# Performance work log

Hardware: AMD Instinct MI355X
Metric: run time of the kernel (lower is better)

Reference implementation:

```python
import jax, jax.numpy as jnp
import numpy as np

D_MODEL = 1024
NUM_HEADS = 16
DEPTH = D_MODEL // NUM_HEADS  # 64
BATCH, SEQ = 4, 2048


def setup_inputs() -> dict:
    key = jax.random.key(0)
    ks = jax.random.split(key, 9)
    s = 1.0 / np.sqrt(D_MODEL)
    x = jax.random.normal(ks[0], (BATCH, SEQ, D_MODEL), dtype=jnp.float32)
    # Per-head Dense weights stacked on a leading head axis [H, d_model, depth]
    Wq = jax.random.normal(ks[1], (NUM_HEADS, D_MODEL, DEPTH), dtype=jnp.float32) * s
    Wk = jax.random.normal(ks[2], (NUM_HEADS, D_MODEL, DEPTH), dtype=jnp.float32) * s
    Wv = jax.random.normal(ks[3], (NUM_HEADS, D_MODEL, DEPTH), dtype=jnp.float32) * s
    bq = jnp.zeros((NUM_HEADS, DEPTH), dtype=jnp.float32)
    bk = jnp.zeros((NUM_HEADS, DEPTH), dtype=jnp.float32)
    bv = jnp.zeros((NUM_HEADS, DEPTH), dtype=jnp.float32)
    Wo = jax.random.normal(ks[4], (D_MODEL, D_MODEL), dtype=jnp.float32) * s
    bo = jnp.zeros((D_MODEL,), dtype=jnp.float32)
    return {"x": x, "Wq": Wq, "bq": bq, "Wk": Wk, "bk": bk,
            "Wv": Wv, "bv": bv, "Wo": Wo, "bo": bo}


def reference(x, Wq, bq, Wk, bk, Wv, bv, Wo, bo):
    # Batched equivalent of the per-head loop: project, attend, concat heads.
    q = jnp.einsum('bsd,hde->bhse', x, Wq) + bq[:, None, :]  # [B,H,S,depth]
    k = jnp.einsum('bsd,hde->bhse', x, Wk) + bk[:, None, :]
    v = jnp.einsum('bsd,hde->bhse', x, Wv) + bv[:, None, :]
    scale = 1.0 / jnp.sqrt(jnp.asarray(DEPTH, dtype=x.dtype))
    scores = jnp.einsum('bhse,bhte->bhst', q, k) * scale      # [B,H,S,S]
    weights = jax.nn.softmax(scores, axis=-1)
    heads = jnp.einsum('bhst,bhte->bhse', weights, v)         # [B,H,S,depth]
    # concat head outputs along last axis in head order (tf.concat axis=-1)
    multi = jnp.transpose(heads, (0, 2, 1, 3)).reshape(x.shape[0], x.shape[1], D_MODEL)
    return multi @ Wo + bo
```

## Files before the change

kernel.cpp:

```cpp
#include <hip/hip_runtime.h>
#include <hip/hip_bf16.h>

#define BATCH 4
#define SEQ   2048
#define DM    1024
#define NH    16
#define DEPTH 64
#define ROWS  (BATCH*SEQ)
#define NQKV  (3*DM)
#define BH    (BATCH*NH)

typedef __attribute__((ext_vector_type(8))) short bf16x8;
typedef __attribute__((ext_vector_type(4))) float f32x4;
typedef __attribute__((ext_vector_type(16))) float f32x16;
typedef unsigned short u16;
typedef unsigned int   u32;

__device__ __forceinline__ u16 f2bf(float f) {
    union { float f; unsigned u; } v; v.f = f;
    unsigned r = v.u + 0x7fff + ((v.u >> 16) & 1);
    return (u16)(r >> 16);
}

__device__ __forceinline__ u32 pk2bf(float a, float b) {
#if __has_builtin(__builtin_amdgcn_cvt_pk_bf16_f32)
    typedef __attribute__((ext_vector_type(2))) __bf16 v2bf;
    union { v2bf v; u32 u; } u_;
    u_.v = __builtin_amdgcn_cvt_pk_bf16_f32(a, b);
    return u_.u;
#else
    return (u32)f2bf(a) | ((u32)f2bf(b) << 16);
#endif
}

__device__ __forceinline__ void plswap(u32 a, u32 b, u32& x, u32& y) {
#if __has_builtin(__builtin_amdgcn_permlane32_swap)
    typedef __attribute__((ext_vector_type(2))) int i32x2;
    i32x2 r = __builtin_amdgcn_permlane32_swap((int)a, (int)b, false, false);
    x = (u32)r.x; y = (u32)r.y;
#else
    u32 as = (u32)__shfl_xor((int)a, 32);
    u32 bs = (u32)__shfl_xor((int)b, 32);
    int h = (threadIdx.x >> 5) & 1;
    x = h ? bs : a;
    y = h ? b : as;
#endif
}

__device__ __forceinline__ void g2l16(void* lds, const void* g) {
    __builtin_amdgcn_global_load_lds((const __attribute__((address_space(1))) void*)g,
                                     (__attribute__((address_space(3))) void*)lds, 16, 0, 0);
}

__device__ __forceinline__ bf16x8 frag8(const u16* tile, int row, int gl) {
    return *(const bf16x8*)(tile + row * 64 + ((gl ^ (row & 7)) * 8));
}

__device__ __forceinline__ f32x16 mfma32(bf16x8 a, bf16x8 b, f32x16 c) {
    return __builtin_amdgcn_mfma_f32_32x32x16_bf16(a, b, c, 0, 0, 0);
}

__global__ __launch_bounds__(256) void k_prep(const float* __restrict__ x,
                                              const float* __restrict__ Wq, const float* __restrict__ Wk,
                                              const float* __restrict__ Wv, const float* __restrict__ Wo,
                                              u16* __restrict__ xb, u16* __restrict__ BT, u16* __restrict__ WoT) {
    __shared__ u16 T[64][65];
    int tid = threadIdx.x;
    int bx = blockIdx.x;
    if (bx < 2048) {
        int i = bx * 4096 + tid * 4;
        for (int l = 0; l < 4; ++l) {
            float4 v = *(const float4*)(x + i + l * 1024);
            ushort4 o; o.x = f2bf(v.x); o.y = f2bf(v.y); o.z = f2bf(v.z); o.w = f2bf(v.w);
            *(ushort4*)(xb + i + l * 1024) = o;
        }
        return;
    }
    if (bx < 2816) {
        int q = bx - 2048;
        int kt = q & 15, mh = q >> 4, m = mh >> 4, h = mh & 15;
        const float* W = (m == 0) ? Wq : (m == 1) ? Wk : Wv;
        const float* src = W + ((size_t)h * 1024 + kt * 64) * 64;
        int e = tid & 63, r0 = tid >> 6;
        for (int i = 0; i < 16; ++i) { int r = i * 4 + r0; T[r][e] = f2bf(src[r * 64 + e]); }
        __syncthreads();
        int kk = tid & 63, e0 = tid >> 6;
        u16* dst = BT + ((size_t)m * 1024 + h * 64) * 1024 + kt * 64;
        for (int i = 0; i < 16; ++i) { int ee = i * 4 + e0; dst[ee * 1024 + kk] = T[kk][ee]; }
        return;
    }
    {
        int q = bx - 2816;
        int kt = q & 15, nt = q >> 4;
        const float* src = Wo + (size_t)kt * 64 * 1024 + nt * 64;
        int c = tid & 63, r0 = tid >> 6;
        for (int i = 0; i < 16; ++i) { int r = i * 4 + r0; T[r][c] = f2bf(src[r * 1024 + c]); }
        __syncthreads();
        int kk = tid & 63, e0 = tid >> 6;
        u16* dst = WoT + (size_t)nt * 64 * 1024 + kt * 64;
        for (int i = 0; i < 16; ++i) { int ee = i * 4 + e0; dst[ee * 1024 + kk] = T[kk][ee]; }
    }
}

__global__ __launch_bounds__(256, 2) void k_gemm_qkv(const u16* __restrict__ xb, const u16* __restrict__ Wt,
                                                     const float* __restrict__ bq, const float* __restrict__ bk,
                                                     const float* __restrict__ bv,
                                                     u16* __restrict__ Q, u16* __restrict__ K, u16* __restrict__ VT) {
    __shared__ u16 Al[2][128 * 64];
    __shared__ u16 Bl[2][128 * 64];
    int tid = threadIdx.x;
    int wave = tid >> 6, lane = tid & 63, l31 = lane & 31, h2 = lane >> 5;
    int wr = wave >> 1, wc = wave & 1;

    int b = blockIdx.x;
    int wg = (b & 7) * 192 + (b >> 3);

    bool isvt = (wg >= 1024);
    int row0, col0;
    const u16 *Am, *Bm;
    if (!isvt) {
        row0 = (wg >> 4) * 128; col0 = (wg & 15) * 128;
        Am = xb + (size_t)row0 * 1024;
        Bm = Wt + (size_t)col0 * 1024;
    } else {
        int b2 = wg - 1024;
        row0 = (b2 >> 6) * 128; col0 = (b2 & 63) * 128;
        Am = Wt + (size_t)(2048 + row0) * 1024;
        Bm = xb + (size_t)col0 * 1024;
    }

    f32x16 acc[2][2] = {};

    int sr[4], sgs[4], sdst[4];
#pragma unroll
    for (int l = 0; l < 4; ++l) {
        int idx = tid + l * 256;
        sr[l] = idx >> 3; sgs[l] = ((idx & 7) ^ (sr[l] & 7)) * 8; sdst[l] = idx * 8;
    }

#define QKV_STAGE(bufi, k0) \
    { _Pragma("unroll") for (int l = 0; l < 4; ++l) { \
        g2l16(&Al[bufi][sdst[l]], Am + sr[l] * 1024 + (k0) + sgs[l]); \
        g2l16(&Bl[bufi][sdst[l]], Bm + sr[l] * 1024 + (k0) + sgs[l]); } }

#define QKV_COMPUTE(bufi) \
    { _Pragma("unroll") for (int kk = 0; kk < 4; ++kk) { \
        bf16x8 a_[2], bb_[2]; \
        _Pragma("unroll") for (int mi = 0; mi < 2; ++mi) a_[mi] = frag8(Al[bufi], wr * 64 + mi * 32 + l31, 2 * kk + h2); \
        _Pragma("unroll") for (int ni = 0; ni < 2; ++ni) bb_[ni] = frag8(Bl[bufi], wc * 64 + ni * 32 + l31, 2 * kk + h2); \
        _Pragma("unroll") for (int mi = 0; mi < 2; ++mi) \
        _Pragma("unroll") for (int ni = 0; ni < 2; ++ni) \
            acc[mi][ni] = mfma32(a_[mi], bb_[ni], acc[mi][ni]); } }

    QKV_STAGE(0, 0)
    QKV_STAGE(1, 64)

    for (int t = 0; t < 15; ++t) {
        int cur = t & 1;
        asm volatile("s_waitcnt vmcnt(8)" ::: "memory");
        __builtin_amdgcn_s_barrier();
        asm volatile("" ::: "memory");
        __builtin_amdgcn_s_setprio(1);
        QKV_COMPUTE(cur)
        __builtin_amdgcn_s_setprio(0);
        asm volatile("" ::: "memory");
        __builtin_amdgcn_s_barrier();
        if (t < 14) QKV_STAGE(cur, (t + 2) * 64)
    }
    asm volatile("s_waitcnt vmcnt(0)" ::: "memory");
    __builtin_amdgcn_s_barrier();
    asm volatile("" ::: "memory");
    QKV_COMPUTE(1)
#undef QKV_STAGE
#undef QKV_COMPUTE

    if (!isvt) {
        const float QSCALE = 0.125f * 1.4426950408889634f;
        int m = (col0 >= 1024);
        const float* bias = m ? bk : bq;
        u16* dst0 = m ? K : Q;
#pragma unroll
        for (int ni = 0; ni < 2; ++ni) {
            int c = col0 + wc * 64 + ni * 32 + l31;
            int h = (c >> 6) & 15, e = c & 63;
            float bval = bias[h * 64 + e];
#pragma unroll
            for (int mi = 0; mi < 2; ++mi)
#pragma unroll
                for (int reg = 0; reg < 16; ++reg) {
                    int rowg = row0 + wr * 64 + mi * 32 + (reg & 3) + 8 * (reg >> 2) + 4 * h2;
                    int b_ = rowg >> 11, s = rowg & 2047;
                    int bh = b_ * 16 + h;
                    float v = acc[mi][ni][reg] + bval;
                    if (!m) v *= QSCALE;
                    dst0[((size_t)bh * 2048 + s) * 64 + e] = f2bf(v);
                }
        }
    } else {
#pragma unroll
        for (int ni = 0; ni < 2; ++ni) {
            int c = col0 + wc * 64 + ni * 32 + l31;
            int b_ = c >> 11, s = c & 2047;
#pragma unroll
            for (int mi = 0; mi < 2; ++mi)
#pragma unroll
                for (int reg = 0; reg < 16; ++reg) {
                    int ii = row0 + wr * 64 + mi * 32 + (reg & 3) + 8 * (reg >> 2) + 4 * h2;
                    float v = acc[mi][ni][reg] + bv[ii];
                    VT[((size_t)b_ * 1024 + ii) * 2048 + s] = f2bf(v);
                }
        }
    }
}

__global__ __launch_bounds__(256, 4) void k_attn(const u16* __restrict__ Q, const u16* __restrict__ K,
                                                 const u16* __restrict__ VT, u16* __restrict__ A2) {
    __shared__ u16 Kl[2][64 * 64];
    __shared__ u16 Vl[2][64 * 64];
    __shared__ float linv[128];
    int tid = threadIdx.x;
    int wave = tid >> 6, lane = tid & 63, l31 = lane & 31, h = lane >> 5;
    int bh = blockIdx.y;
    int m0 = blockIdx.x * 128;
    const u16* Qb = Q + (size_t)bh * 2048 * 64;
    const u16* Kb = K + (size_t)bh * 2048 * 64;
    const u16* Vb = VT + (size_t)bh * 64 * 2048;

    const u16* kp[2]; const u16* vp[2]; int dsti[2];
    for (int l = 0; l < 2; ++l) {
        int idx = tid + l * 256, r = idx >> 3, gs = ((idx & 7) ^ (r & 7)) * 8;
        dsti[l] = idx * 8;
        kp[l] = Kb + r * 64 + gs;
        vp[l] = Vb + r * 2048 + gs;
    }

    bf16x8 qb[4];
    {
        const u16* q0 = Qb + (size_t)(m0 + wave * 32 + l31) * 64 + h * 8;
#pragma unroll
        for (int s = 0; s < 4; ++s) qb[s] = *(const bf16x8*)(q0 + s * 16);
    }

    for (int l = 0; l < 2; ++l) { g2l16(&Kl[0][dsti[l]], kp[l]); g2l16(&Vl[0][dsti[l]], vp[l]); }
    asm volatile("s_waitcnt vmcnt(0)" ::: "memory");
    __builtin_amdgcn_s_barrier();
    asm volatile("" ::: "memory");

    f32x16 oacc[2] = {};
    float lsum = 0.f;
    bf16x8 pa[4] = {};

    for (int t = 0; t < 32; ++t) {
        int cur = t & 1, nxt = cur ^ 1;

        if (t < 31) {
            for (int l = 0; l < 2; ++l) g2l16(&Kl[nxt][dsti[l]], kp[l] + (t + 1) * 4096);
        }

        f32x16 sc[2] = {};
        __builtin_amdgcn_s_setprio(1);
#pragma unroll
        for (int s = 0; s < 4; ++s) {
            bf16x8 kf0 = frag8(Kl[cur], l31,      2 * s + h);
            bf16x8 kf1 = frag8(Kl[cur], 32 + l31, 2 * s + h);
            sc[0] = mfma32(kf0, qb[s], sc[0]);
            sc[1] = mfma32(kf1, qb[s], sc[1]);
        }
        if (t > 0) {
#pragma unroll
            for (int s = 0; s < 4; ++s) {
                bf16x8 bv0 = frag8(Vl[nxt], l31,      2 * s + h);
                bf16x8 bv1 = frag8(Vl[nxt], 32 + l31, 2 * s + h);
                oacc[0] = mfma32(pa[s], bv0, oacc[0]);
                oacc[1] = mfma32(pa[s], bv1, oacc[1]);
            }
        }
        __builtin_amdgcn_s_setprio(0);

        asm volatile("" ::: "memory");
        __builtin_amdgcn_s_barrier();
        asm volatile("" ::: "memory");

        if (t < 31) {
            for (int l = 0; l < 2; ++l) g2l16(&Vl[nxt][dsti[l]], vp[l] + (t + 1) * 64);
        }

        float sq = 0.f;
#pragma unroll
        for (int kt = 0; kt < 2; ++kt)
#pragma unroll
            for (int gp = 0; gp < 2; ++gp) {
                float e00 = __builtin_amdgcn_exp2f(sc[kt][(2 * gp) * 4 + 0]);
                float e01 = __builtin_amdgcn_exp2f(sc[kt][(2 * gp) * 4 + 1]);
                float e02 = __builtin_amdgcn_exp2f(sc[kt][(2 * gp) * 4 + 2]);
                float e03 = __builtin_amdgcn_exp2f(sc[kt][(2 * gp) * 4 + 3]);
                float e10 = __builtin_amdgcn_exp2f(sc[kt][(2 * gp + 1) * 4 + 0]);
                float e11 = __builtin_amdgcn_exp2f(sc[kt][(2 * gp + 1) * 4 + 1]);
                float e12 = __builtin_amdgcn_exp2f(sc[kt][(2 * gp + 1) * 4 + 2]);
                float e13 = __builtin_amdgcn_exp2f(sc[kt][(2 * gp + 1) * 4 + 3]);
                sq += ((e00 + e01) + (e02 + e03)) + ((e10 + e11) + (e12 + e13));
                u32 ue = pk2bf(e00, e01), ve = pk2bf(e02, e03);
                u32 uo = pk2bf(e10, e11), vo = pk2bf(e12, e13);
                u32 w0, w1, w2, w3;
                plswap(ue, uo, w0, w2);
                plswap(ve, vo, w1, w3);
                union { bf16x8 v; u32 w[4]; } pu;
                pu.w[0] = w0; pu.w[1] = w1; pu.w[2] = w2; pu.w[3] = w3;
                pa[2 * kt + gp] = pu.v;
            }
        lsum += sq;

        if (t < 31) {
            asm volatile("s_waitcnt vmcnt(0)" ::: "memory");
            __builtin_amdgcn_s_barrier();
            asm volatile("" ::: "memory");
        }
    }

#pragma unroll
    for (int s = 0; s < 4; ++s) {
        bf16x8 bv0 = frag8(Vl[1], l31,      2 * s + h);
        bf16x8 bv1 = frag8(Vl[1], 32 + l31, 2 * s + h);
        oacc[0] = mfma32(pa[s], bv0, oacc[0]);
        oacc[1] = mfma32(pa[s], bv1, oacc[1]);
    }

    {
        float l2 = lsum + __shfl_xor(lsum, 32);
        linv[wave * 32 + l31] = 1.0f / l2;
    }
    int b_ = bh >> 4, hh = bh & 15;
    for (int g = 0; g < 4; ++g) {
        f32x4 iv = *(f32x4*)&linv[wave * 32 + 8 * g + 4 * h];
        for (int dt = 0; dt < 2; ++dt)
            for (int r = 0; r < 4; ++r) {
                int row = b_ * 2048 + m0 + wave * 32 + 8 * g + 4 * h + r;
                A2[row * 1024 + hh * 64 + dt * 32 + l31] = f2bf(oacc[dt][g * 4 + r] * iv[r]);
            }
    }
}

__global__ __launch_bounds__(256, 2) void k_gemm_out(const u16* __restrict__ A, const u16* __restrict__ BT,
                                                     const float* __restrict__ bo, float* __restrict__ out) {
    __shared__ u16 Al[2][128 * 64];
    __shared__ u16 Bl[2][128 * 64];
    int tid = threadIdx.x;
    int wave = tid >> 6, lane = tid & 63, l31 = lane & 31, h2 = lane >> 5;
    int wr = wave >> 1, wc = wave & 1;

    int b = blockIdx.x;
    int wg = (b & 7) * 64 + (b >> 3);
    int row0 = (wg >> 3) * 128, col0 = (wg & 7) * 128;

    const u16* Am = A  + (size_t)row0 * 1024;
    const u16* Bm = BT + (size_t)col0 * 1024;

    f32x16 acc[2][2] = {};

    int sr[4], sgs[4], sdst[4];
#pragma unroll
    for (int l = 0; l < 4; ++l) {
        int idx = tid + l * 256;
        sr[l] = idx >> 3; sgs[l] = ((idx & 7) ^ (sr[l] & 7)) * 8; sdst[l] = idx * 8;
    }

#define OUT_STAGE(bufi, k0) \
    { _Pragma("unroll") for (int l = 0; l < 4; ++l) { \
        g2l16(&Al[bufi][sdst[l]], Am + sr[l] * 1024 + (k0) + sgs[l]); \
        g2l16(&Bl[bufi][sdst[l]], Bm + sr[l] * 1024 + (k0) + sgs[l]); } }

#define OUT_COMPUTE(bufi) \
    { _Pragma("unroll") for (int kk = 0; kk < 4; ++kk) { \
        bf16x8 a_[2], bb_[2]; \
        _Pragma("unroll") for (int mi = 0; mi < 2; ++mi) a_[mi] = frag8(Al[bufi], wr * 64 + mi * 32 + l31, 2 * kk + h2); \
        _Pragma("unroll") for (int ni = 0; ni < 2; ++ni) bb_[ni] = frag8(Bl[bufi], wc * 64 + ni * 32 + l31, 2 * kk + h2); \
        _Pragma("unroll") for (int mi = 0; mi < 2; ++mi) \
        _Pragma("unroll") for (int ni = 0; ni < 2; ++ni) \
            acc[mi][ni] = mfma32(a_[mi], bb_[ni], acc[mi][ni]); } }

    OUT_STAGE(0, 0)
    OUT_STAGE(1, 64)

    for (int t = 0; t < 15; ++t) {
        int cur = t & 1;
        asm volatile("s_waitcnt vmcnt(8)" ::: "memory");
        __builtin_amdgcn_s_barrier();
        asm volatile("" ::: "memory");
        __builtin_amdgcn_s_setprio(1);
        OUT_COMPUTE(cur)
        __builtin_amdgcn_s_setprio(0);
        asm volatile("" ::: "memory");
        __builtin_amdgcn_s_barrier();
        if (t < 14) OUT_STAGE(cur, (t + 2) * 64)
    }
    asm volatile("s_waitcnt vmcnt(0)" ::: "memory");
    __builtin_amdgcn_s_barrier();
    asm volatile("" ::: "memory");
    OUT_COMPUTE(1)
#undef OUT_STAGE
#undef OUT_COMPUTE

#pragma unroll
    for (int ni = 0; ni < 2; ++ni) {
        int c = col0 + wc * 64 + ni * 32 + l31;
        float bias = bo[c];
#pragma unroll
        for (int mi = 0; mi < 2; ++mi)
#pragma unroll
            for (int reg = 0; reg < 16; ++reg) {
                int rowg = row0 + wr * 64 + mi * 32 + (reg & 3) + 8 * (reg >> 2) + 4 * h2;
                out[(size_t)rowg * 1024 + c] = acc[mi][ni][reg] + bias;
            }
    }
}

extern "C" void kernel_launch(void* const* d_in, const int* in_sizes, int n_in,
                              void* d_out, int out_size, void* d_ws, size_t ws_size,
                              hipStream_t stream) {
    const float* x  = (const float*)d_in[0];
    const float* Wq = (const float*)d_in[1];
    const float* bq = (const float*)d_in[2];
    const float* Wk = (const float*)d_in[3];
    const float* bk = (const float*)d_in[4];
    const float* Wv = (const float*)d_in[5];
    const float* bv = (const float*)d_in[6];
    const float* Wo = (const float*)d_in[7];
    const float* bo = (const float*)d_in[8];
    float* out = (float*)d_out;

    char* ws = (char*)d_ws;
    u16* xb    = (u16*)ws; ws += (size_t)ROWS * DM * 2;
    u16* WqkvT = (u16*)ws; ws += (size_t)NQKV * DM * 2;
    u16* WoT   = (u16*)ws; ws += (size_t)DM * DM * 2;
    u16* Qb    = (u16*)ws; ws += (size_t)BH * SEQ * DEPTH * 2;
    u16* Kb    = (u16*)ws; ws += (size_t)BH * SEQ * DEPTH * 2;
    u16* VTb   = (u16*)ws; ws += (size_t)BH * SEQ * DEPTH * 2;
    u16* A2    = xb;
    (void)ws_size;

    k_prep     <<<dim3(3072),   dim3(256), 0, stream>>>(x, Wq, Wk, Wv, Wo, xb, WqkvT, WoT);
    k_gemm_qkv <<<dim3(1536),   dim3(256), 0, stream>>>(xb, WqkvT, bq, bk, bv, Qb, Kb, VTb);
    k_attn     <<<dim3(16, 64), dim3(256), 0, stream>>>(Qb, Kb, VTb, A2);
    k_gemm_out <<<dim3(512),    dim3(256), 0, stream>>>(A2, WoT, bo, out);
}
```

Measured before the change: 289.8 us.

## Triple-buffer V tiles in attention to drop mid-iteration barrier, remap blocks

```diff
diff --git a/kernel.cpp b/kernel.cpp
--- a/kernel.cpp
+++ b/kernel.cpp
@@ -216,12 +216,12 @@
 __global__ __launch_bounds__(256, 4) void k_attn(const u16* __restrict__ Q, const u16* __restrict__ K,
                                                  const u16* __restrict__ VT, u16* __restrict__ A2) {
     __shared__ u16 Kl[2][64 * 64];
-    __shared__ u16 Vl[2][64 * 64];
-    __shared__ float linv[128];
+    __shared__ u16 Vl[3][64 * 64];
     int tid = threadIdx.x;
     int wave = tid >> 6, lane = tid & 63, l31 = lane & 31, h = lane >> 5;
-    int bh = blockIdx.y;
-    int m0 = blockIdx.x * 128;
+    int i = blockIdx.x;
+    int bh = (i & 7) * 8 + ((i >> 3) & 7);
+    int m0 = (i >> 6) * 128;
     const u16* Qb = Q + (size_t)bh * 2048 * 64;
     const u16* Kb = K + (size_t)bh * 2048 * 64;
     const u16* Vb = VT + (size_t)bh * 64 * 2048;
@@ -249,12 +249,17 @@
     f32x16 oacc[2] = {};
     float lsum = 0.f;
     bf16x8 pa[4] = {};
+    int vw = 1;
+    int vr = 2;
 
     for (int t = 0; t < 32; ++t) {
         int cur = t & 1, nxt = cur ^ 1;
 
         if (t < 31) {
-            for (int l = 0; l < 2; ++l) g2l16(&Kl[nxt][dsti[l]], kp[l] + (t + 1) * 4096);
+            for (int l = 0; l < 2; ++l) {
+                g2l16(&Kl[nxt][dsti[l]], kp[l] + (t + 1) * 4096);
+                g2l16(&Vl[vw][dsti[l]], vp[l] + (t + 1) * 64);
+            }
         }
 
         f32x16 sc[2] = {};
@@ -267,23 +272,16 @@
             sc[1] = mfma32(kf1, qb[s], sc[1]);
         }
         if (t > 0) {
+            const u16* vt_ = Vl[vr];
 #pragma unroll
             for (int s = 0; s < 4; ++s) {
-                bf16x8 bv0 = frag8(Vl[nxt], l31,      2 * s + h);
-                bf16x8 bv1 = frag8(Vl[nxt], 32 + l31, 2 * s + h);
+                bf16x8 bv0 = frag8(vt_, l31,      2 * s + h);
+                bf16x8 bv1 = frag8(vt_, 32 + l31, 2 * s + h);
                 oacc[0] = mfma32(pa[s], bv0, oacc[0]);
                 oacc[1] = mfma32(pa[s], bv1, oacc[1]);
             }
         }
         __builtin_amdgcn_s_setprio(0);
-
-        asm volatile("" ::: "memory");
-        __builtin_amdgcn_s_barrier();
-        asm volatile("" ::: "memory");
-
-        if (t < 31) {
-            for (int l = 0; l < 2; ++l) g2l16(&Vl[nxt][dsti[l]], vp[l] + (t + 1) * 64);
-        }
 
         float sq = 0.f;
 #pragma unroll
@@ -315,6 +313,8 @@
             __builtin_amdgcn_s_barrier();
             asm volatile("" ::: "memory");
         }
+        vw = (vw == 2) ? 0 : vw + 1;
+        vr = (vr == 2) ? 0 : vr + 1;
     }
 
 #pragma unroll
@@ -325,18 +325,20 @@
         oacc[1] = mfma32(pa[s], bv1, oacc[1]);
     }
 
+    float linv_own;
     {
         float l2 = lsum + __shfl_xor(lsum, 32);
-        linv[wave * 32 + l31] = 1.0f / l2;
+        linv_own = 1.0f / l2;
     }
     int b_ = bh >> 4, hh = bh & 15;
     for (int g = 0; g < 4; ++g) {
-        f32x4 iv = *(f32x4*)&linv[wave * 32 + 8 * g + 4 * h];
-        for (int dt = 0; dt < 2; ++dt)
-            for (int r = 0; r < 4; ++r) {
-                int row = b_ * 2048 + m0 + wave * 32 + 8 * g + 4 * h + r;
-                A2[row * 1024 + hh * 64 + dt * 32 + l31] = f2bf(oacc[dt][g * 4 + r] * iv[r]);
-            }
+#pragma unroll
+        for (int r = 0; r < 4; ++r) {
+            float iv = __shfl(linv_own, 8 * g + 4 * h + r);
+            int row = b_ * 2048 + m0 + wave * 32 + 8 * g + 4 * h + r;
+            for (int dt = 0; dt < 2; ++dt)
+                A2[row * 1024 + hh * 64 + dt * 32 + l31] = f2bf(oacc[dt][g * 4 + r] * iv);
+        }
     }
 }
 
@@ -440,6 +442,6 @@
 
     k_prep     <<<dim3(3072),   dim3(256), 0, stream>>>(x, Wq, Wk, Wv, Wo, xb, WqkvT, WoT);
     k_gemm_qkv <<<dim3(1536),   dim3(256), 0, stream>>>(xb, WqkvT, bq, bk, bv, Qb, Kb, VTb);
-    k_attn     <<<dim3(16, 64), dim3(256), 0, stream>>>(Qb, Kb, VTb, A2);
+    k_attn     <<<dim3(1024),   dim3(256), 0, stream>>>(Qb, Kb, VTb, A2);
     k_gemm_out <<<dim3(512),    dim3(256), 0, stream>>>(A2, WoT, bo, out);
 }
```

Measured after the change: 285.5 us. Within noise of the previous version (-1.5%).
